# Kernel optimization log

Hardware: AMD Instinct MI355X
Metric: run time of the kernel (lower is better)

## Reference

```python
import jax, jax.numpy as jnp
import numpy as np

NUM_TOKENS = 16384
NUM_HEADS = 8
HEAD_SIZE = 128
NUM_BLOCKS = 4096
BLOCK_SIZE = 16
NUM_SLOTS = NUM_BLOCKS * BLOCK_SIZE


def setup_inputs() -> dict:
    key = jax.random.key(0)
    k1, k2, k3, k4, k5 = jax.random.split(key, 5)
    # Unique, in-range slots (random permutation) so the scatter is deterministic.
    slot_mapping = jax.random.permutation(k5, NUM_SLOTS)[:NUM_TOKENS].astype(jnp.int64)
    return {
        "key": jax.random.normal(k1, (NUM_TOKENS, NUM_HEADS, HEAD_SIZE), dtype=jnp.float32),
        "value": jax.random.normal(k2, (NUM_TOKENS, NUM_HEADS, HEAD_SIZE), dtype=jnp.float32),
        "key_cache": jax.random.normal(k3, (NUM_BLOCKS, BLOCK_SIZE, NUM_HEADS, HEAD_SIZE), dtype=jnp.float32),
        "value_cache": jax.random.normal(k4, (NUM_BLOCKS, BLOCK_SIZE, NUM_HEADS, HEAD_SIZE), dtype=jnp.float32),
        "slot_mapping": slot_mapping,
        "k_scale": jnp.ones((1,), dtype=jnp.float32),
        "v_scale": jnp.ones((1,), dtype=jnp.float32),
    }


def reference(key, value, key_cache, value_cache, slot_mapping, k_scale, v_scale):
    # kv_cache_dtype='auto' in the torch Model, so FP8_KV_CACHE is False and
    # k_scale/v_scale are never applied. The op is a pure paged scatter:
    #   cache[slot // block_size, slot % block_size] = token  (skip slot < 0)
    num_blocks, block_size = key_cache.shape[0], key_cache.shape[1]
    num_slots = num_blocks * block_size
    # View caches as flat slot-major [num_slots, heads, head_size].
    kc_flat = key_cache.reshape(num_slots, *key_cache.shape[2:])
    vc_flat = value_cache.reshape(num_slots, *value_cache.shape[2:])
    # Redirect negative slots out-of-range; mode='drop' skips those writes.
    safe_slot = jnp.where(slot_mapping < 0, num_slots, slot_mapping)
    kc_flat = kc_flat.at[safe_slot].set(key, mode="drop")
    vc_flat = vc_flat.at[safe_slot].set(value, mode="drop")
    return (kc_flat.reshape(key_cache.shape), vc_flat.reshape(value_cache.shape))
```

## Files before the change

kernel.cpp:

```cpp
#include <hip/hip_runtime.h>

#define NUM_TOKENS   16384
#define NUM_HEADS    8
#define HEAD_SIZE    128
#define NUM_BLOCKS   4096
#define BLOCK_SIZE_  16
#define SLOT_ELEMS   (NUM_HEADS * HEAD_SIZE)
#define SLOT_VEC4    (SLOT_ELEMS / 4)
#define NUM_SLOTS    (NUM_BLOCKS * BLOCK_SIZE_)
#define CACHE_ELEMS  ((long)NUM_SLOTS * SLOT_ELEMS)

typedef float f4_t __attribute__((ext_vector_type(4)));
__device__ __forceinline__ void nt_store(float4* p, float4 v) {
    __builtin_nontemporal_store(*(f4_t*)&v, (f4_t*)p);
}
__device__ __forceinline__ float4 nt_load(const float4* p) {
    f4_t v = __builtin_nontemporal_load((const f4_t*)p);
    return *(float4*)&v;
}

__global__ void build_inverse_kernel(const int* __restrict__ slot_mapping,
                                     int* __restrict__ inv) {
    int t = blockIdx.x * blockDim.x + threadIdx.x;
    if (t < NUM_TOKENS) {
        int s = slot_mapping[t];
        if (s >= 0) inv[s] = t;
    }
}

__global__ __launch_bounds__(256)
void scatter_kv_kernel(const float4* __restrict__ key,
                       const float4* __restrict__ value,
                       const int* __restrict__ slot_mapping,
                       float4* __restrict__ ok,
                       float4* __restrict__ ov) {
    int token = blockIdx.x;
    int slot = slot_mapping[token];
    if (slot < 0) return;
    int tid = threadIdx.x;
    long src = (long)token * SLOT_VEC4 + tid;
    long dst = (long)slot  * SLOT_VEC4 + tid;
    float4 rk = nt_load(key + src);
    float4 rv = nt_load(value + src);
    nt_store(ok + dst, rk);
    nt_store(ov + dst, rv);
}

__global__ __launch_bounds__(256)
void copy_holes_kernel(const float4* __restrict__ kc,
                       const float4* __restrict__ vc,
                       const int* __restrict__ inv,
                       float4* __restrict__ ok,
                       float4* __restrict__ ov) {
    int slot = blockIdx.x;
    if (inv[slot] >= 0) return;
    long i = (long)slot * SLOT_VEC4 + threadIdx.x;
    float4 rk = nt_load(kc + i);
    float4 rv = nt_load(vc + i);
    nt_store(ok + i, rk);
    nt_store(ov + i, rv);
}


__global__ void copy_cache_kernel(const float4* __restrict__ kc,
                                  const float4* __restrict__ vc,
                                  float4* __restrict__ ok,
                                  float4* __restrict__ ov,
                                  long n4) {
    long i = (long)blockIdx.x * blockDim.x + threadIdx.x;
    long stride = (long)gridDim.x * blockDim.x;
    for (; i < n4; i += stride) {
        ok[i] = kc[i];
        ov[i] = vc[i];
    }
}

extern "C" void kernel_launch(void* const* d_in, const int* in_sizes, int n_in,
                              void* d_out, int out_size, void* d_ws, size_t ws_size,
                              hipStream_t stream) {
    const float* key   = (const float*)d_in[0];
    const float* value = (const float*)d_in[1];
    const float* kc    = (const float*)d_in[2];
    const float* vc    = (const float*)d_in[3];
    const int*   slots = (const int*)d_in[4];

    float* ok = (float*)d_out;
    float* ov = ok + CACHE_ELEMS;

    if (ws_size >= (size_t)NUM_SLOTS * sizeof(int)) {
        int* inv = (int*)d_ws;
        hipMemsetAsync(inv, 0xFF, NUM_SLOTS * sizeof(int), stream);
        build_inverse_kernel<<<(NUM_TOKENS + 255) / 256, 256, 0, stream>>>(slots, inv);
        copy_holes_kernel<<<NUM_SLOTS, 256, 0, stream>>>(
            (const float4*)kc, (const float4*)vc, inv, (float4*)ok, (float4*)ov);
        scatter_kv_kernel<<<NUM_TOKENS, 256, 0, stream>>>(
            (const float4*)key, (const float4*)value, slots, (float4*)ok, (float4*)ov);
    } else {
        long n4 = CACHE_ELEMS / 4;
        copy_cache_kernel<<<2048, 256, 0, stream>>>(
            (const float4*)kc, (const float4*)vc, (float4*)ok, (float4*)ov, n4);
        scatter_kv_kernel<<<NUM_TOKENS, 256, 0, stream>>>(
            (const float4*)key, (const float4*)value, slots, (float4*)ok, (float4*)ov);
    }
}
```

Before: 200.8 us.

## Fuse inverse-map build into scatter and batch hole copies four slots per block

Removes the separate inverse-building kernel by having the scatter kernel record each token's slot in the inverse map while it copies the token data. The hole-copy kernel now runs after the scatter and handles four slots per block, reading the inverse entries as one int4. This drops one launch and cuts the hole-copy grid by four, at the cost of a serial dependency where hole copies must wait for the scatter to finish. The old scatter kernel is re-added without nontemporal hints for the fallback path.

Measured after the change: 204.1 us. About the same (+1.6%).

```diff
diff --git a/kernel.cpp b/kernel.cpp
--- a/kernel.cpp
+++ b/kernel.cpp
@@ -19,24 +19,17 @@
     return *(float4*)&v;
 }
 
-__global__ void build_inverse_kernel(const int* __restrict__ slot_mapping,
-                                     int* __restrict__ inv) {
-    int t = blockIdx.x * blockDim.x + threadIdx.x;
-    if (t < NUM_TOKENS) {
-        int s = slot_mapping[t];
-        if (s >= 0) inv[s] = t;
-    }
-}
-
 __global__ __launch_bounds__(256)
-void scatter_kv_kernel(const float4* __restrict__ key,
-                       const float4* __restrict__ value,
-                       const int* __restrict__ slot_mapping,
-                       float4* __restrict__ ok,
-                       float4* __restrict__ ov) {
+void scatter_build_kernel(const float4* __restrict__ key,
+                          const float4* __restrict__ value,
+                          const int* __restrict__ slot_mapping,
+                          int* __restrict__ inv,
+                          float4* __restrict__ ok,
+                          float4* __restrict__ ov) {
     int token = blockIdx.x;
     int slot = slot_mapping[token];
     if (slot < 0) return;
+    if (threadIdx.x == 0) inv[slot] = token;
     int tid = threadIdx.x;
     long src = (long)token * SLOT_VEC4 + tid;
     long dst = (long)slot  * SLOT_VEC4 + tid;
@@ -47,18 +40,26 @@
 }
 
 __global__ __launch_bounds__(256)
-void copy_holes_kernel(const float4* __restrict__ kc,
-                       const float4* __restrict__ vc,
-                       const int* __restrict__ inv,
-                       float4* __restrict__ ok,
-                       float4* __restrict__ ov) {
-    int slot = blockIdx.x;
-    if (inv[slot] >= 0) return;
-    long i = (long)slot * SLOT_VEC4 + threadIdx.x;
-    float4 rk = nt_load(kc + i);
-    float4 rv = nt_load(vc + i);
-    nt_store(ok + i, rk);
-    nt_store(ov + i, rv);
+void copy_holes4_kernel(const float4* __restrict__ kc,
+                        const float4* __restrict__ vc,
+                        const int4* __restrict__ inv4,
+                        float4* __restrict__ ok,
+                        float4* __restrict__ ov) {
+    int s0 = blockIdx.x * 4;
+    int4 iv = inv4[blockIdx.x];
+    int tid = threadIdx.x;
+    long base = (long)s0 * SLOT_VEC4 + tid;
+#pragma unroll
+    for (int j = 0; j < 4; ++j) {
+        int tok = (j == 0) ? iv.x : (j == 1) ? iv.y : (j == 2) ? iv.z : iv.w;
+        if (tok < 0) {
+            long i = base + (long)j * SLOT_VEC4;
+            float4 rk = nt_load(kc + i);
+            float4 rv = nt_load(vc + i);
+            nt_store(ok + i, rk);
+            nt_store(ov + i, rv);
+        }
+    }
 }
 
 
@@ -73,6 +74,21 @@
         ok[i] = kc[i];
         ov[i] = vc[i];
     }
+}
+
+__global__ void scatter_kv_kernel(const float4* __restrict__ key,
+                                  const float4* __restrict__ value,
+                                  const int* __restrict__ slot_mapping,
+                                  float4* __restrict__ ok,
+                                  float4* __restrict__ ov) {
+    int token = blockIdx.x;
+    int slot = slot_mapping[token];
+    if (slot < 0) return;
+    int tid = threadIdx.x;
+    long src = (long)token * SLOT_VEC4 + tid;
+    long dst = (long)slot  * SLOT_VEC4 + tid;
+    ok[dst] = key[src];
+    ov[dst] = value[src];
 }
 
 extern "C" void kernel_launch(void* const* d_in, const int* in_sizes, int n_in,
@@ -90,11 +106,12 @@
     if (ws_size >= (size_t)NUM_SLOTS * sizeof(int)) {
         int* inv = (int*)d_ws;
         hipMemsetAsync(inv, 0xFF, NUM_SLOTS * sizeof(int), stream);
-        build_inverse_kernel<<<(NUM_TOKENS + 255) / 256, 256, 0, stream>>>(slots, inv);
-        copy_holes_kernel<<<NUM_SLOTS, 256, 0, stream>>>(
-            (const float4*)kc, (const float4*)vc, inv, (float4*)ok, (float4*)ov);
-        scatter_kv_kernel<<<NUM_TOKENS, 256, 0, stream>>>(
-            (const float4*)key, (const float4*)value, slots, (float4*)ok, (float4*)ov);
+        scatter_build_kernel<<<NUM_TOKENS, 256, 0, stream>>>(
+            (const float4*)key, (const float4*)value, slots, inv,
+            (float4*)ok, (float4*)ov);
+        copy_holes4_kernel<<<NUM_SLOTS / 4, 256, 0, stream>>>(
+            (const float4*)kc, (const float4*)vc, (const int4*)inv,
+            (float4*)ok, (float4*)ov);
     } else {
         long n4 = CACHE_ELEMS / 4;
         copy_cache_kernel<<<2048, 256, 0, stream>>>(
```
